# Performance work log

Measured on AMD Instinct MI355X. Metric: run time of the kernel, lower is better.

## Reference

```python
import jax, jax.numpy as jnp
import numpy as np

B, T, C, H, HS = 128, 256, 384, 6, 64
DFF = 4 * C
EPS = 1e-5


def layer_norm(x, g, b):
    mu = jnp.mean(x, axis=-1, keepdims=True)
    var = jnp.mean(jnp.square(x - mu), axis=-1, keepdims=True)
    return (x - mu) * jax.lax.rsqrt(var + EPS) * g + b


def setup_inputs() -> dict:
    key = jax.random.key(0)
    ks = jax.random.split(key, 12)
    s_in = 1.0 / np.sqrt(C)
    s_ff = 1.0 / np.sqrt(DFF)
    return {
        "x": jax.random.normal(ks[0], (B, T, C), jnp.float32),
        "Wq": jax.random.normal(ks[1], (H, C, HS), jnp.float32) * s_in,
        "Wk": jax.random.normal(ks[2], (H, C, HS), jnp.float32) * s_in,
        "Wv": jax.random.normal(ks[3], (H, C, HS), jnp.float32) * s_in,
        "Wo": jax.random.normal(ks[4], (C, C), jnp.float32) * s_in,
        "bo": jnp.zeros((C,), jnp.float32),
        "W1": jax.random.normal(ks[5], (C, DFF), jnp.float32) * s_in,
        "b1": jnp.zeros((DFF,), jnp.float32),
        "W2": jax.random.normal(ks[6], (DFF, C), jnp.float32) * s_ff,
        "b2": jnp.zeros((C,), jnp.float32),
        "g1": jnp.ones((C,), jnp.float32),
        "be1": jnp.zeros((C,), jnp.float32),
        "g2": jnp.ones((C,), jnp.float32),
        "be2": jnp.zeros((C,), jnp.float32),
    }


def reference(x, Wq, Wk, Wv, Wo, bo, W1, b1, W2, b2, g1, be1, g2, be2):
    # --- pre-norm causal multi-head self-attention (dropout = identity, eval mode) ---
    h = layer_norm(x, g1, be1)                      # (B,T,C)
    q = jnp.einsum('btc,hcd->bhtd', h, Wq)          # (B,H,T,HS)
    k = jnp.einsum('btc,hcd->bhtd', h, Wk)
    v = jnp.einsum('btc,hcd->bhtd', h, Wv)
    scale = HS ** -0.5
    wei = jnp.einsum('bhtd,bhsd->bhts', q, k) * scale   # (B,H,T,T)
    causal = jnp.tril(jnp.ones((T, T), bool))
    wei = jnp.where(causal, wei, -jnp.inf)
    wei = jax.nn.softmax(wei, axis=-1)
    attn = jnp.einsum('bhts,bhsd->bhtd', wei, v)         # (B,H,T,HS)
    attn = attn.transpose(0, 2, 1, 3).reshape(x.shape[0], x.shape[1], C)  # concat heads
    sa = attn @ Wo + bo
    x = x + sa
    # --- pre-norm FFN ---
    h2 = layer_norm(x, g2, be2)
    ff = jax.nn.relu(h2 @ W1 + b1) @ W2 + b2
    return x + ff
```

## Files before the change

### kernel.cpp

```cpp
#include <hip/hip_runtime.h>
#include <hip/hip_bf16.h>

#define BB   128
#define TT   256
#define CC   384
#define HH   6
#define HSZ  64
#define DFF  1536
#define EPSV 1e-5f
#define RPB  8
#define NTOK (BB * TT)
#define NQKV (3 * CC)

typedef __attribute__((ext_vector_type(8))) short  short8;
typedef __attribute__((ext_vector_type(4))) float  f32x4;
typedef __hip_bfloat16 bf16;

__device__ __forceinline__ void async_copy16(const bf16* g, bf16* l) {
    __builtin_amdgcn_global_load_lds(
        (const __attribute__((address_space(1))) void*)g,
        (__attribute__((address_space(3))) void*)l, 16, 0, 0);
}

__device__ __forceinline__ void block_reduce2(float& a, float& b, float* red) {
    #pragma unroll
    for (int off = 32; off > 0; off >>= 1) {
        a += __shfl_down(a, off, 64);
        b += __shfl_down(b, off, 64);
    }
    const int lane = threadIdx.x & 63;
    const int wid  = threadIdx.x >> 6;
    if (lane == 0) { red[wid * 2] = a; red[wid * 2 + 1] = b; }
    __syncthreads();
    if (threadIdx.x == 0) {
        float sa = 0.f, sb = 0.f;
        #pragma unroll
        for (int w = 0; w < 6; ++w) { sa += red[w * 2]; sb += red[w * 2 + 1]; }
        red[12] = sa; red[13] = sb;
    }
    __syncthreads();
    a = red[12]; b = red[13];
}

__global__ __launch_bounds__(CC) void ln_bf16_kernel(
        const float* __restrict__ x, const float* __restrict__ g,
        const float* __restrict__ be, bf16* __restrict__ y) {
    __shared__ float red[16];
    const int tid = threadIdx.x;
    const long row0 = (long)blockIdx.x * RPB;
    const float gg = g[tid], bb = be[tid];
    for (int r = 0; r < RPB; ++r) {
        float v = x[(row0 + r) * CC + tid];
        float s = v, sq = v * v;
        block_reduce2(s, sq, red);
        float mu  = s  * (1.0f / CC);
        float var = sq * (1.0f / CC) - mu * mu;
        float rs  = rsqrtf(var + EPSV);
        y[(row0 + r) * CC + tid] = __float2bfloat16((v - mu) * rs * gg + bb);
        __syncthreads();
    }
}

__global__ __launch_bounds__(256) void pack_weights(
        const float* __restrict__ Wq, const float* __restrict__ Wk,
        const float* __restrict__ Wv, const float* __restrict__ Wo,
        const float* __restrict__ W1, const float* __restrict__ W2,
        bf16* __restrict__ WcatT, bf16* __restrict__ WoT,
        bf16* __restrict__ W1T, bf16* __restrict__ W2T) {
    __shared__ float t[32][33];
    const int id = blockIdx.x;
    const float* in; bf16* out; int R, Cn, c0, r0;
    if (id < 432) {
        const int which = id / 144, rem = id % 144, h = rem / 24, tt = rem % 24;
        const float* W = (which == 0) ? Wq : ((which == 1) ? Wk : Wv);
        in = W + (long)h * CC * HSZ;  R = CC; Cn = HSZ;
        c0 = (tt % 2) * 32; r0 = (tt / 2) * 32;
        out = WcatT + ((long)which * CC + h * HSZ) * CC;
    } else if (id < 576) {
        const int i2 = id - 432;
        in = Wo; out = WoT; R = CC; Cn = CC;
        c0 = (i2 % 12) * 32; r0 = (i2 / 12) * 32;
    } else if (id < 1152) {
        const int i3 = id - 576;
        in = W1; out = W1T; R = CC; Cn = DFF;
        c0 = (i3 % 48) * 32; r0 = (i3 / 48) * 32;
    } else {
        const int i4 = id - 1152;
        in = W2; out = W2T; R = DFF; Cn = CC;
        c0 = (i4 % 12) * 32; r0 = (i4 / 12) * 32;
    }
    const int tid = threadIdx.x, tx = tid & 31, ty = tid >> 5;
    #pragma unroll
    for (int p = 0; p < 4; ++p)
        t[ty + p * 8][tx] = in[(long)(r0 + ty + p * 8) * Cn + c0 + tx];
    __syncthreads();
    #pragma unroll
    for (int p = 0; p < 4; ++p)
        out[(long)(c0 + ty + p * 8) * R + r0 + tx] = __float2bfloat16(t[tx][ty + p * 8]);
}

template<int K, int EPI>
__global__ __launch_bounds__(256) void gemm_bt(
        const bf16* __restrict__ A, const bf16* __restrict__ BT,
        const float* __restrict__ bias, const float* __restrict__ res,
        float* __restrict__ outF, bf16* __restrict__ outB, int N, int nby) {
    __shared__ bf16 A0[128 * 32];
    __shared__ bf16 A1[128 * 32];
    __shared__ bf16 A2[128 * 32];
    __shared__ bf16 B0[128 * 32];
    __shared__ bf16 B1[128 * 32];
    __shared__ bf16 B2[128 * 32];

    const int tid = threadIdx.x;

    const int hwid  = blockIdx.x;
    const int chunk = gridDim.x >> 3;
    const int e     = hwid & 7;
    const int s     = hwid >> 3;
    const int gx    = chunk / nby;
    const int bx    = e * gx + s / nby;
    const int by    = s - (s / nby) * nby;
    const int m0 = bx * 128;
    const int n0 = by * 128;

    const int ln   = tid & 63;
    const int wid  = tid >> 6;
    const int wm   = (wid & 1) * 64;
    const int wn   = (wid >> 1) * 64;
    const int fr   = ln & 15;
    const int quad = ln >> 4;
    const int slot = quad ^ ((fr >> 1) & 3);

    const int u0 = tid, u1 = tid + 256;
    const int r0c = u0 >> 2, g0 = (u0 & 3) ^ ((r0c >> 1) & 3);
    const int r1c = u1 >> 2, g1 = (u1 & 3) ^ ((r1c >> 1) & 3);
    const long ga0 = (long)r0c * K + g0 * 8;
    const long ga1 = (long)r1c * K + g1 * 8;
    const bf16* Ap  = A  + (long)m0 * K;
    const bf16* BTp = BT + (long)n0 * K;

    f32x4 acc[4][4];
    #pragma unroll
    for (int i = 0; i < 4; ++i)
        #pragma unroll
        for (int j = 0; j < 4; ++j)
            acc[i][j] = (f32x4){0.f, 0.f, 0.f, 0.f};

    constexpr int NT = K / 32;
    static_assert(NT % 3 == 0, "3-phase rotation requires NT % 3 == 0");

    auto stage = [&](long k0, bf16* Ad, bf16* Bd) {
        async_copy16(Ap  + ga0 + k0, Ad + u0 * 8);
        async_copy16(Ap  + ga1 + k0, Ad + u1 * 8);
        async_copy16(BTp + ga0 + k0, Bd + u0 * 8);
        async_copy16(BTp + ga1 + k0, Bd + u1 * 8);
    };

    auto phase = [&](int t, const bf16* Ac, const bf16* Bc, bf16* Astg, bf16* Bstg) {
        if (t + 1 < NT) {
            asm volatile("s_waitcnt vmcnt(4)" ::: "memory");
        } else {
            asm volatile("s_waitcnt vmcnt(0)" ::: "memory");
        }
        asm volatile("s_waitcnt lgkmcnt(0)" ::: "memory");
        __builtin_amdgcn_s_barrier();
        __builtin_amdgcn_sched_barrier(0);

        if (t + 2 < NT) stage((long)(t + 2) * 32, Astg, Bstg);

        short8 af[4], bfr[4];
        #pragma unroll
        for (int i = 0; i < 4; ++i) {
            const int R = wm + i * 16 + fr;
            af[i] = *(const short8*)(Ac + R * 32 + slot * 8);
        }
        #pragma unroll
        for (int j = 0; j < 4; ++j) {
            const int R = wn + j * 16 + fr;
            bfr[j] = *(const short8*)(Bc + R * 32 + slot * 8);
        }
        #pragma unroll
        for (int i = 0; i < 4; ++i)
            #pragma unroll
            for (int j = 0; j < 4; ++j)
                acc[i][j] = __builtin_amdgcn_mfma_f32_16x16x32_bf16(
                    af[i], bfr[j], acc[i][j], 0, 0, 0);
    };

    stage(0,  A0, B0);
    stage(32, A1, B1);

    for (int tb = 0; tb < NT; tb += 3) {
        phase(tb,     A0, B0, A2, B2);
        phase(tb + 1, A1, B1, A0, B0);
        phase(tb + 2, A2, B2, A1, B1);
    }

    #pragma unroll
    for (int i = 0; i < 4; ++i) {
        #pragma unroll
        for (int j = 0; j < 4; ++j) {
            const int col = n0 + wn + j * 16 + fr;
            #pragma unroll
            for (int r = 0; r < 4; ++r) {
                const int row = m0 + wm + i * 16 + quad * 4 + r;
                const long idx = (long)row * N + col;
                float v = acc[i][j][r];
                if (EPI == 1) {
                    v = fmaxf(v + bias[col], 0.f);
                    outB[idx] = __float2bfloat16(v);
                } else if (EPI == 2) {
                    outF[idx] = v + bias[col] + res[idx];
                } else {
                    outB[idx] = __float2bfloat16(v);
                }
            }
        }
    }
}

struct alignas(8) bh4s { bf16 a, b, c, d; };

__global__ __launch_bounds__(256, 2) void attn_mfma_kernel(
        const bf16* __restrict__ qkv, bf16* __restrict__ ab) {
    __shared__ bf16 Kt[64][72];
    __shared__ bf16 Vt[64][72];
    __shared__ bf16 Pb[4][16][72];

    const int tid  = threadIdx.x;
    const int bh   = blockIdx.x;
    const int b    = bh / HH, h = bh % HH;
    const int w    = tid >> 6;
    const int ln   = tid & 63;
    const int ln15 = ln & 15;
    const int quad = ln >> 4;

    short8 qf[4][2];
    #pragma unroll
    for (int i = 0; i < 4; ++i) {
        const long tok = (long)b * TT + w * 16 + i * 64 + ln15;
        const bf16* p = qkv + tok * NQKV + h * HSZ + quad * 8;
        qf[i][0] = *(const short8*)p;
        qf[i][1] = *(const short8*)(p + 32);
    }

    f32x4 accO[4][4];
    float mrow[4][4], lrow[4][4];
    #pragma unroll
    for (int i = 0; i < 4; ++i) {
        #pragma unroll
        for (int j = 0; j < 4; ++j) accO[i][j] = (f32x4){0.f, 0.f, 0.f, 0.f};
        #pragma unroll
        for (int r = 0; r < 4; ++r) { mrow[i][r] = -1e30f; lrow[i][r] = 0.f; }
    }

    for (int sidx = 0; sidx < 4; ++sidx) {
        const int s0 = sidx * 64;
        __syncthreads();
        {
            const bf16* kg = qkv + (long)(b * TT + s0) * NQKV + CC + h * HSZ;
            #pragma unroll
            for (int it = 0; it < 2; ++it) {
                const int u = tid + it * 256;
                const int r = u >> 3, c = (u & 7) * 8;
                *(uint4*)&Kt[r][c] = *(const uint4*)(kg + (long)r * NQKV + c);
            }
            const bf16* vg = qkv + (long)(b * TT + s0) * NQKV + 2 * CC + h * HSZ;
            const int s = tid & 63;
            #pragma unroll
            for (int it = 0; it < 4; ++it) {
                const int dq = (tid >> 6) + it * 4;
                const bh4s vv = *(const bh4s*)(vg + (long)s * NQKV + dq * 4);
                Vt[dq * 4 + 0][s] = vv.a;
                Vt[dq * 4 + 1][s] = vv.b;
                Vt[dq * 4 + 2][s] = vv.c;
                Vt[dq * 4 + 3][s] = vv.d;
            }
        }
        __syncthreads();

        #pragma unroll
        for (int i = 0; i < 4; ++i) {
            if (i < sidx) continue;
            const int rb = w * 16 + i * 64;
            f32x4 S[4];
            #pragma unroll
            for (int jt = 0; jt < 4; ++jt) S[jt] = (f32x4){0.f, 0.f, 0.f, 0.f};
            #pragma unroll
            for (int ks = 0; ks < 2; ++ks) {
                #pragma unroll
                for (int jt = 0; jt < 4; ++jt) {
                    const short8 kf = *(const short8*)&Kt[jt * 16 + ln15][ks * 32 + quad * 8];
                    S[jt] = __builtin_amdgcn_mfma_f32_16x16x32_bf16(qf[i][ks], kf, S[jt], 0, 0, 0);
                }
            }
            float rmax[4];
            #pragma unroll
            for (int r = 0; r < 4; ++r) rmax[r] = -1e30f;
            #pragma unroll
            for (int jt = 0; jt < 4; ++jt) {
                #pragma unroll
                for (int r = 0; r < 4; ++r) {
                    float v = S[jt][r] * 0.125f;
                    if (i == sidx) {
                        const int col = s0 + jt * 16 + ln15;
                        const int row = rb + quad * 4 + r;
                        if (col > row) v = -1e30f;
                    }
                    S[jt][r] = v;
                    rmax[r] = fmaxf(rmax[r], v);
                }
            }
            #pragma unroll
            for (int off = 1; off < 16; off <<= 1)
                #pragma unroll
                for (int r = 0; r < 4; ++r)
                    rmax[r] = fmaxf(rmax[r], __shfl_xor(rmax[r], off, 64));

            float alpha[4], rsum[4];
            #pragma unroll
            for (int r = 0; r < 4; ++r) {
                const float mn = fmaxf(mrow[i][r], rmax[r]);
                alpha[r] = __expf(mrow[i][r] - mn);
                mrow[i][r] = mn;
                rsum[r] = 0.f;
            }
            #pragma unroll
            for (int jt = 0; jt < 4; ++jt)
                #pragma unroll
                for (int r = 0; r < 4; ++r) {
                    const float p = __expf(S[jt][r] - mrow[i][r]);
                    S[jt][r] = p;
                    rsum[r] += p;
                }
            #pragma unroll
            for (int off = 1; off < 16; off <<= 1)
                #pragma unroll
                for (int r = 0; r < 4; ++r)
                    rsum[r] += __shfl_xor(rsum[r], off, 64);
            #pragma unroll
            for (int r = 0; r < 4; ++r)
                lrow[i][r] = lrow[i][r] * alpha[r] + rsum[r];
            #pragma unroll
            for (int jt = 0; jt < 4; ++jt)
                #pragma unroll
                for (int r = 0; r < 4; ++r)
                    accO[i][jt][r] *= alpha[r];

            #pragma unroll
            for (int jt = 0; jt < 4; ++jt)
                #pragma unroll
                for (int r = 0; r < 4; ++r)
                    Pb[w][quad * 4 + r][jt * 16 + ln15] = __float2bfloat16(S[jt][r]);
            const short8 pf0 = *(const short8*)&Pb[w][ln15][quad * 8];
            const short8 pf1 = *(const short8*)&Pb[w][ln15][32 + quad * 8];
            #pragma unroll
            for (int jt = 0; jt < 4; ++jt) {
                const short8 vf0 = *(const short8*)&Vt[jt * 16 + ln15][quad * 8];
                const short8 vf1 = *(const short8*)&Vt[jt * 16 + ln15][32 + quad * 8];
                accO[i][jt] = __builtin_amdgcn_mfma_f32_16x16x32_bf16(pf0, vf0, accO[i][jt], 0, 0, 0);
                accO[i][jt] = __builtin_amdgcn_mfma_f32_16x16x32_bf16(pf1, vf1, accO[i][jt], 0, 0, 0);
            }
        }
    }

    #pragma unroll
    for (int i = 0; i < 4; ++i) {
        const int rb = w * 16 + i * 64;
        float inv[4];
        #pragma unroll
        for (int r = 0; r < 4; ++r) inv[r] = 1.0f / lrow[i][r];
        #pragma unroll
        for (int jt = 0; jt < 4; ++jt)
            #pragma unroll
            for (int r = 0; r < 4; ++r)
                Pb[w][quad * 4 + r][jt * 16 + ln15] = __float2bfloat16(accO[i][jt][r] * inv[r]);
        #pragma unroll
        for (int it = 0; it < 2; ++it) {
            const int u = ln + it * 64;
            const int row = u >> 3, ch = (u & 7) * 8;
            const long tok = (long)b * TT + rb + row;
            *(uint4*)(ab + tok * CC + h * HSZ + ch) = *(const uint4*)&Pb[w][row][ch];
        }
    }
}

extern "C" void kernel_launch(void* const* d_in, const int* in_sizes, int n_in,
                              void* d_out, int out_size, void* d_ws, size_t ws_size,
                              hipStream_t stream) {
    const float* x   = (const float*)d_in[0];
    const float* Wq  = (const float*)d_in[1];
    const float* Wk  = (const float*)d_in[2];
    const float* Wv  = (const float*)d_in[3];
    const float* Wo  = (const float*)d_in[4];
    const float* bo  = (const float*)d_in[5];
    const float* W1  = (const float*)d_in[6];
    const float* b1  = (const float*)d_in[7];
    const float* W2  = (const float*)d_in[8];
    const float* b2  = (const float*)d_in[9];
    const float* g1  = (const float*)d_in[10];
    const float* be1 = (const float*)d_in[11];
    const float* g2  = (const float*)d_in[12];
    const float* be2 = (const float*)d_in[13];

    float* out = (float*)d_out;
    char*  ws  = (char*)d_ws;

    const size_t qkvBytes = (size_t)NTOK * NQKV * 4;
    const size_t actOff   = (qkvBytes + 255) & ~(size_t)255;
    const size_t actBytes = (size_t)NTOK * CC * 2;
    size_t wOff = (actOff + actBytes + 255) & ~(size_t)255;

    bf16* qkvb = (bf16*)ws;
    bf16* ff1  = (bf16*)ws;
    bf16* actb = (bf16*)(ws + actOff);

    bf16* WcatT = (bf16*)(ws + wOff); wOff += (size_t)NQKV * CC * 2 + 256;
    bf16* WoT   = (bf16*)(ws + ((wOff + 255) & ~(size_t)255)); wOff = ((wOff + 255) & ~(size_t)255) + (size_t)CC * CC * 2;
    bf16* W1T   = (bf16*)(ws + ((wOff + 255) & ~(size_t)255)); wOff = ((wOff + 255) & ~(size_t)255) + (size_t)DFF * CC * 2;
    bf16* W2T   = (bf16*)(ws + ((wOff + 255) & ~(size_t)255));

    pack_weights<<<1728, 256, 0, stream>>>(Wq, Wk, Wv, Wo, W1, W2,
                                           WcatT, WoT, W1T, W2T);

    ln_bf16_kernel<<<NTOK / RPB, CC, 0, stream>>>(x, g1, be1, actb);
    gemm_bt<CC, 3><<<(NTOK / 128) * (NQKV / 128), 256, 0, stream>>>(
        actb, WcatT, nullptr, nullptr, nullptr, qkvb, NQKV, NQKV / 128);
    attn_mfma_kernel<<<BB * HH, 256, 0, stream>>>(qkvb, actb);
    gemm_bt<CC, 2><<<(NTOK / 128) * (CC / 128), 256, 0, stream>>>(
        actb, WoT, bo, x, out, nullptr, CC, CC / 128);

    ln_bf16_kernel<<<NTOK / RPB, CC, 0, stream>>>(out, g2, be2, actb);
    gemm_bt<CC, 1><<<(NTOK / 128) * (DFF / 128), 256, 0, stream>>>(
        actb, W1T, b1, nullptr, nullptr, ff1, DFF, DFF / 128);
    gemm_bt<DFF, 2><<<(NTOK / 128) * (CC / 128), 256, 0, stream>>>(
        ff1, W2T, b2, out, out, nullptr, CC, CC / 128);
}
```

Before: 411.0 us.

## Widen GEMM tiles to 128x384 with 512 threads and double buffering

The GEMM kernel now computes 128x384 output tiles with 8 waves (512 threads), each wave holding a 64x96 accumulator block, instead of 128x128 tiles with 4 waves. The LDS pipeline goes from three stages to two, and LDS fragment reads now happen before a second barrier so a buffer can be refilled safely. The aim is more reuse of each A tile across a wider N and fewer blocks, at the cost of higher register use per thread, two barriers per k-step and shallower prefetch. Grids shrink sharply, for example to 256 blocks for the N=384 GEMMs, which may leave CUs underused.

```diff
diff --git a/kernel.cpp b/kernel.cpp
--- a/kernel.cpp
+++ b/kernel.cpp
@@ -100,16 +100,14 @@
 }
 
 template<int K, int EPI>
-__global__ __launch_bounds__(256) void gemm_bt(
+__global__ __launch_bounds__(512) void gemm_fn(
         const bf16* __restrict__ A, const bf16* __restrict__ BT,
         const float* __restrict__ bias, const float* __restrict__ res,
         float* __restrict__ outF, bf16* __restrict__ outB, int N, int nby) {
     __shared__ bf16 A0[128 * 32];
     __shared__ bf16 A1[128 * 32];
-    __shared__ bf16 A2[128 * 32];
-    __shared__ bf16 B0[128 * 32];
-    __shared__ bf16 B1[128 * 32];
-    __shared__ bf16 B2[128 * 32];
+    __shared__ bf16 B0[384 * 32];
+    __shared__ bf16 B1[384 * 32];
 
     const int tid = threadIdx.x;
 
@@ -121,68 +119,70 @@
     const int bx    = e * gx + s / nby;
     const int by    = s - (s / nby) * nby;
     const int m0 = bx * 128;
-    const int n0 = by * 128;
+    const int n0 = by * 384;
 
     const int ln   = tid & 63;
     const int wid  = tid >> 6;
     const int wm   = (wid & 1) * 64;
-    const int wn   = (wid >> 1) * 64;
+    const int wn   = (wid >> 1) * 96;
     const int fr   = ln & 15;
     const int quad = ln >> 4;
     const int slot = quad ^ ((fr >> 1) & 3);
 
-    const int u0 = tid, u1 = tid + 256;
-    const int r0c = u0 >> 2, g0 = (u0 & 3) ^ ((r0c >> 1) & 3);
-    const int r1c = u1 >> 2, g1 = (u1 & 3) ^ ((r1c >> 1) & 3);
-    const long ga0 = (long)r0c * K + g0 * 8;
-    const long ga1 = (long)r1c * K + g1 * 8;
+    const int rA = tid >> 2, gA = (tid & 3) ^ ((rA >> 1) & 3);
+    const long gaA = (long)rA * K + gA * 8;
+    const int uB1 = tid + 512, uB2 = tid + 1024;
+    const int rB0 = tid >> 2, gB0 = (tid & 3) ^ ((rB0 >> 1) & 3);
+    const int rB1 = uB1 >> 2, gB1 = (uB1 & 3) ^ ((rB1 >> 1) & 3);
+    const int rB2 = uB2 >> 2, gB2 = (uB2 & 3) ^ ((rB2 >> 1) & 3);
+    const long gaB0 = (long)rB0 * K + gB0 * 8;
+    const long gaB1 = (long)rB1 * K + gB1 * 8;
+    const long gaB2 = (long)rB2 * K + gB2 * 8;
     const bf16* Ap  = A  + (long)m0 * K;
     const bf16* BTp = BT + (long)n0 * K;
 
-    f32x4 acc[4][4];
+    f32x4 acc[4][6];
     #pragma unroll
     for (int i = 0; i < 4; ++i)
         #pragma unroll
-        for (int j = 0; j < 4; ++j)
+        for (int j = 0; j < 6; ++j)
             acc[i][j] = (f32x4){0.f, 0.f, 0.f, 0.f};
 
     constexpr int NT = K / 32;
-    static_assert(NT % 3 == 0, "3-phase rotation requires NT % 3 == 0");
+    static_assert(NT % 2 == 0, "2-buffer rotation requires even NT");
 
     auto stage = [&](long k0, bf16* Ad, bf16* Bd) {
-        async_copy16(Ap  + ga0 + k0, Ad + u0 * 8);
-        async_copy16(Ap  + ga1 + k0, Ad + u1 * 8);
-        async_copy16(BTp + ga0 + k0, Bd + u0 * 8);
-        async_copy16(BTp + ga1 + k0, Bd + u1 * 8);
+        async_copy16(Ap  + gaA  + k0, Ad + tid * 8);
+        async_copy16(BTp + gaB0 + k0, Bd + tid * 8);
+        async_copy16(BTp + gaB1 + k0, Bd + uB1 * 8);
+        async_copy16(BTp + gaB2 + k0, Bd + uB2 * 8);
     };
 
-    auto phase = [&](int t, const bf16* Ac, const bf16* Bc, bf16* Astg, bf16* Bstg) {
+    auto phase = [&](int t, bf16* Ab, bf16* Bb) {
         if (t + 1 < NT) {
             asm volatile("s_waitcnt vmcnt(4)" ::: "memory");
         } else {
             asm volatile("s_waitcnt vmcnt(0)" ::: "memory");
         }
+        __builtin_amdgcn_s_barrier();
+
+        short8 af[4], bfr[6];
+        #pragma unroll
+        for (int i = 0; i < 4; ++i)
+            af[i] = *(const short8*)(Ab + (wm + i * 16 + fr) * 32 + slot * 8);
+        #pragma unroll
+        for (int j = 0; j < 6; ++j)
+            bfr[j] = *(const short8*)(Bb + (wn + j * 16 + fr) * 32 + slot * 8);
         asm volatile("s_waitcnt lgkmcnt(0)" ::: "memory");
         __builtin_amdgcn_s_barrier();
         __builtin_amdgcn_sched_barrier(0);
 
-        if (t + 2 < NT) stage((long)(t + 2) * 32, Astg, Bstg);
-
-        short8 af[4], bfr[4];
-        #pragma unroll
-        for (int i = 0; i < 4; ++i) {
-            const int R = wm + i * 16 + fr;
-            af[i] = *(const short8*)(Ac + R * 32 + slot * 8);
-        }
-        #pragma unroll
-        for (int j = 0; j < 4; ++j) {
-            const int R = wn + j * 16 + fr;
-            bfr[j] = *(const short8*)(Bc + R * 32 + slot * 8);
-        }
+        if (t + 2 < NT) stage((long)(t + 2) * 32, Ab, Bb);
+
         #pragma unroll
         for (int i = 0; i < 4; ++i)
             #pragma unroll
-            for (int j = 0; j < 4; ++j)
+            for (int j = 0; j < 6; ++j)
                 acc[i][j] = __builtin_amdgcn_mfma_f32_16x16x32_bf16(
                     af[i], bfr[j], acc[i][j], 0, 0, 0);
     };
@@ -190,16 +190,15 @@
     stage(0,  A0, B0);
     stage(32, A1, B1);
 
-    for (int tb = 0; tb < NT; tb += 3) {
-        phase(tb,     A0, B0, A2, B2);
-        phase(tb + 1, A1, B1, A0, B0);
-        phase(tb + 2, A2, B2, A1, B1);
+    for (int t = 0; t < NT; t += 2) {
+        phase(t,     A0, B0);
+        phase(t + 1, A1, B1);
     }
 
     #pragma unroll
     for (int i = 0; i < 4; ++i) {
         #pragma unroll
-        for (int j = 0; j < 4; ++j) {
+        for (int j = 0; j < 6; ++j) {
             const int col = n0 + wn + j * 16 + fr;
             #pragma unroll
             for (int r = 0; r < 4; ++r) {
@@ -424,15 +423,15 @@
                                            WcatT, WoT, W1T, W2T);
 
     ln_bf16_kernel<<<NTOK / RPB, CC, 0, stream>>>(x, g1, be1, actb);
-    gemm_bt<CC, 3><<<(NTOK / 128) * (NQKV / 128), 256, 0, stream>>>(
-        actb, WcatT, nullptr, nullptr, nullptr, qkvb, NQKV, NQKV / 128);
+    gemm_fn<CC, 3><<<(NTOK / 128) * 3, 512, 0, stream>>>(
+        actb, WcatT, nullptr, nullptr, nullptr, qkvb, NQKV, 3);
     attn_mfma_kernel<<<BB * HH, 256, 0, stream>>>(qkvb, actb);
-    gemm_bt<CC, 2><<<(NTOK / 128) * (CC / 128), 256, 0, stream>>>(
-        actb, WoT, bo, x, out, nullptr, CC, CC / 128);
+    gemm_fn<CC, 2><<<(NTOK / 128), 512, 0, stream>>>(
+        actb, WoT, bo, x, out, nullptr, CC, 1);
 
     ln_bf16_kernel<<<NTOK / RPB, CC, 0, stream>>>(out, g2, be2, actb);
-    gemm_bt<CC, 1><<<(NTOK / 128) * (DFF / 128), 256, 0, stream>>>(
-        actb, W1T, b1, nullptr, nullptr, ff1, DFF, DFF / 128);
-    gemm_bt<DFF, 2><<<(NTOK / 128) * (CC / 128), 256, 0, stream>>>(
-        ff1, W2T, b2, out, out, nullptr, CC, CC / 128);
-}
+    gemm_fn<CC, 1><<<(NTOK / 128) * 4, 512, 0, stream>>>(
+        actb, W1T, b1, nullptr, nullptr, ff1, DFF, 4);
+    gemm_fn<DFF, 2><<<(NTOK / 128), 512, 0, stream>>>(
+        ff1, W2T, b2, out, out, nullptr, CC, 1);
+}
```

Result: no change. 412.9 us (+0.5%).
